# Optimization experiments

Measured on AMD Instinct MI355X. Metric: run time of the kernel, lower is better.

## Reference

```python
import jax, jax.numpy as jnp
import numpy as np

D = 20       # bond_dim (= virtual_dim = per-module output_dim)
BATCH = 128
BN_EPS = 1e-5


def _unfold(t, h, w, n):
    # torch x.unfold(2,h,h).unfold(3,w,w).reshape(b, C, -1, n)
    B, C, H, W = t.shape
    t = t.reshape(B, C, H // h, h, W // w, w).transpose(0, 1, 2, 4, 3, 5)
    return t.reshape(B, C, -1, n)


def _mps(x, cores, label):
    # x: [b, C, P, n] site values; cores: [P, n, D, F, D] with F = 2*C; label: [P, D, O, D]
    feat = jnp.concatenate([x, 1.0 - x], axis=1)              # [b, F, P, n]  ([x, 1-x] feature map)
    M = jnp.einsum('bfpn,pnufv->npbuv', feat, cores)           # [n, P, b, D, D] site matrices
    v = jnp.full((cores.shape[2],), cores.shape[2] ** -0.5, dtype=x.dtype)  # boundary vector
    left = jnp.einsum('u,pbuv->pbv', v, M[0])
    for i in range(1, M.shape[0]):                             # n is small & static (4 or 16)
        left = jnp.einsum('pbu,pbuv->pbv', left, M[i])
    return jnp.einsum('pbu,puov,v->bpo', left, label, v)       # [b, P, O]


def _bn(y, gamma, beta):
    # training-mode BatchNorm1d over channel axis 1 of [b, C, L]
    mean = y.mean(axis=(0, 2), keepdims=True)
    var = y.var(axis=(0, 2), keepdims=True)
    return (y - mean) * jax.lax.rsqrt(var + BN_EPS) * gamma[None, :, None] + beta[None, :, None]


def setup_inputs() -> dict:
    key = jax.random.key(0)
    ks = jax.random.split(key, 9)
    f32 = jnp.float32
    def core(k, shape):
        F = shape[-2]
        return (jax.random.normal(k, shape, f32) * np.float32(np.sqrt(3.0 / (D * F))))
    def lab(k, shape):
        return jax.random.normal(k, shape, f32) * np.float32(D ** -0.5)
    x = jax.random.uniform(ks[0], (BATCH, 48, 32, 32), f32)
    return {
        'x': x,
        'cores1': core(ks[1], (256, 4, D, 96, D)), 'label1': lab(ks[2], (256, D, D, D)),
        'g1': jnp.ones(256, f32), 'b1': jnp.zeros(256, f32),
        'cores2': core(ks[3], (64, 4, D, 2 * D, D)), 'label2': lab(ks[4], (64, D, D, D)),
        'g2': jnp.ones(64, f32), 'b2': jnp.zeros(64, f32),
        'cores3': core(ks[5], (16, 4, D, 2 * D, D)), 'label3': lab(ks[6], (16, D, D, D)),
        'g3': jnp.ones(16, f32), 'b3': jnp.zeros(16, f32),
        'coresF': core(ks[7], (16, D, 2 * D, D)), 'labelF': lab(ks[8], (D, 10, D)),
    }


def reference(x, cores1, label1, g1, b1, cores2, label2, g2, b2,
              cores3, label3, g3, b3, coresF, labelF):
    b = x.shape[0]
    # stage 1: 256 patch-experts over 4 sites each
    x1 = _unfold(x, 16, 16, 4)                  # [b, 48, 256, 4]
    y = _mps(x1, cores1, label1)                # [b, 256, D]
    y = _bn(y, g1, b1).reshape(b, D, 16, 16)    # faithful patch<->bond mixing view
    # stage 2: 64 experts
    y2 = _unfold(y, 8, 8, 4)                    # [b, D, 64, 4]
    y = _mps(y2, cores2, label2)                # [b, 64, D]
    y = _bn(y, g2, b2).reshape(b, D, 8, 8)
    # stage 3: 16 experts
    y3 = _unfold(y, 4, 4, 4)                    # [b, D, 16, 4]
    y = _mps(y3, cores3, label3)                # [b, 16, D]
    y = _bn(y, g3, b3)
    # final MPS over the 16 expert outputs (channels = D)
    y = y.transpose(0, 2, 1)[:, :, None, :]     # [b, D, 1, 16]
    out = _mps(y, coresF[None], labelF[None])   # [b, 1, 10]
    return out[:, 0, :]                         # squeeze -> [b, 10]
```

## Files before the change

kernel.cpp:

```cpp
#include <hip/hip_runtime.h>

#define VB 0.22360679774997896f

typedef __attribute__((ext_vector_type(8))) _Float16 half8;
typedef __attribute__((ext_vector_type(4))) float f32x4;

#define Z1_OFF   0
#define Z2_OFF   655360
#define Z3_OFF   819200
#define GS1_OFF  860160
#define GQ1_OFF  860416
#define GS2_OFF  860672
#define GQ2_OFF  860736
#define GS3_OFF  860800
#define GQ3_OFF  860816
#define LV1_OFF  860832
#define LV2_OFF  963232
#define LV3_OFF  988832
#define WH2_OFF  995232
#define WH3_OFF  4272032

#define WAVEBAR() __builtin_amdgcn_wave_barrier()

__global__ __launch_bounds__(256, 8)
void prep_kernel(const float* __restrict__ c2, const float* __restrict__ c3,
                 const float* __restrict__ l1, const float* __restrict__ l2,
                 const float* __restrict__ l3,
                 _Float16* __restrict__ Wh2, _Float16* __restrict__ Wh3,
                 float* __restrict__ v1, float* __restrict__ v2,
                 float* __restrict__ v3,
                 float* __restrict__ gzero)
{
    const int tid = threadIdx.x;
    const int b   = blockIdx.x;

    if (b < 4000) {
        int gidx = b * 256 + tid;
        int bb = gidx / 640;
        int o  = gidx - bb * 640;
        const float* src;
        _Float16* dst;
        if (bb < 1280) { src = c2 + (size_t)bb * 3200;          dst = Wh2 + (size_t)bb * 5120; }
        else           { src = c3 + (size_t)(bb - 1280) * 3200; dst = Wh3 + (size_t)(bb - 1280) * 5120; }
        int q  = o >> 6, l = o & 63;
        int ks = q / 5, nt = q - ks * 5;
        int c  = nt * 16 + (l & 15);
        int ul = c / 20;
        int v  = c - ul * 20;
        int f0 = ks * 32 + ((l >> 4) << 3);
        half8 hv;
        if (f0 < 40) {
            const float* sp = src + ul * 800 + f0 * 20 + v;
            #pragma unroll
            for (int j = 0; j < 8; ++j) hv[j] = (_Float16)sp[j * 20];
        } else {
            #pragma unroll
            for (int j = 0; j < 8; ++j) hv[j] = (_Float16)0.f;
        }
        *(half8*)(dst + (size_t)o * 8) = hv;
    } else if (b < 4336) {
        const int bb = b - 4000;
        const float* lb;
        float* ov;
        if (bb < 256)      { lb = l1 + (size_t)bb * 8000;         ov = v1 + bb * 400; }
        else if (bb < 320) { lb = l2 + (size_t)(bb - 256) * 8000; ov = v2 + (bb - 256) * 400; }
        else               { lb = l3 + (size_t)(bb - 320) * 8000; ov = v3 + (bb - 320) * 400; }
        for (int i = tid; i < 400; i += 256) {
            const float4* s = (const float4*)(lb + i * 20);
            float acc = 0.f;
            #pragma unroll
            for (int t = 0; t < 5; ++t) {
                float4 w = s[t];
                acc += w.x + w.y + w.z + w.w;
            }
            ov[i] = acc * VB;
        }
    } else {
        for (int i = tid; i < 672; i += 256) gzero[i] = 0.f;
    }
}

#define CHUNKX(ucv, LAST)                                                     \
    {                                                                         \
        if (!(LAST)) {                                                        \
            _Pragma("unroll")                                                 \
            for (int k = 0; k < 4; ++k) {                                     \
                int i4 = tid + k * 512;                                       \
                if (i4 < 1920) wr[k] = *(const float4*)(wnext + i4 * 4);      \
            }                                                                 \
            wnext += 7680;                                                    \
        }                                                                     \
        f32x4 acc[5];                                                         \
        _Pragma("unroll")                                                     \
        for (int nt = 0; nt < 5; ++nt) acc[nt] = (f32x4){0.f, 0.f, 0.f, 0.f};\
        _Pragma("unroll")                                                     \
        for (int ks = 0; ks < 3; ++ks) {                                      \
            _Pragma("unroll")                                                 \
            for (int nt = 0; nt < 5; ++nt) {                                  \
                half8 bf = *(const half8*)&Fcur[((ks * 5 + nt) * 64 + l) * 8];\
                acc[nt] = __builtin_amdgcn_mfma_f32_16x16x32_f16(             \
                    af[ks], bf, acc[nt], 0, 0, 0);                            \
            }                                                                 \
        }                                                                     \
        _Pragma("unroll")                                                     \
        for (int nt = 0; nt < 5; ++nt) {                                      \
            _Pragma("unroll")                                                 \
            for (int r = 0; r < 4; ++r)                                       \
                Mw[(hi * 4 + r) * 84 + nt * 16 + row16] = acc[nt][r];         \
        }                                                                     \
        WAVEBAR();                                                            \
        _Pragma("unroll")                                                     \
        for (int ul = 0; ul < 4; ++ul) {                                      \
            float lvx = lw[bQ * 20 + (ucv) * 4 + ul];                         \
            _Pragma("unroll")                                                 \
            for (int j = 0; j < 5; ++j)                                       \
                lacc[j] += lvx * Mw[bQ * 84 + ul * 20 + mh * 5 + j];          \
        }                                                                     \
        WAVEBAR();                                                            \
        __syncthreads();                                                      \
        if (!(LAST)) {                                                        \
            _Pragma("unroll")                                                 \
            for (int k = 0; k < 4; ++k) {                                     \
                int i4 = tid + k * 512;                                       \
                if (i4 < 1920) {                                              \
                    float vals[4] = {wr[k].x, wr[k].y, wr[k].z, wr[k].w};     \
                    _Pragma("unroll")                                         \
                    for (int t = 0; t < 4; ++t)                               \
                        Fnxt[sAddr[k][t]] = (_Float16)vals[t];                \
                }                                                             \
            }                                                                 \
        }                                                                     \
        __syncthreads();                                                      \
        { _Float16* t_ = Fcur; Fcur = Fnxt; Fnxt = t_; }                      \
    }

__global__ __launch_bounds__(512, 2)
void fused1_kernel(const float* __restrict__ x, const float* __restrict__ cores1,
                   const float* __restrict__ labv,
                   float* __restrict__ z1, float* __restrict__ gs, float* __restrict__ gq)
{
    __shared__ __align__(16) float xS[8 * 768];
    __shared__ __align__(16) _Float16 Fbuf[2][7680];
    __shared__ __align__(16) float MchunkS[8 * 16 * 84];
    __shared__ __align__(16) float leftS[8 * 320];
    __shared__ float redS[16];

    const int tid = threadIdx.x;
    const int bid = blockIdx.x;
    const int p   = (bid & 7) * 32 + (bid >> 3);
    const int wv  = tid >> 6, l = tid & 63;
    float* xSw = xS + wv * 768;
    float* Mw  = MchunkS + wv * 1344;
    float* lw  = leftS + wv * 320;
    const int row16 = l & 15, hi = l >> 4;
    const int bQ = l >> 2,   mh = l & 3;
    const int hh  = (p >> 7) * 16 + ((p >> 2) & 15);
    const int ww0 = ((p >> 6) & 1) * 16 + (p & 3) * 4;

    float4 xr[12];
    #pragma unroll
    for (int k = 0; k < 12; ++k) {
        int idx = l + k * 64;
        int br = idx / 48, c = idx - br * 48;
        xr[k] = *(const float4*)(x + (((size_t)((wv * 16 + br) * 48 + c)) << 10)
                                   + hh * 32 + ww0);
    }

    int sAddr[4][4];
    #pragma unroll
    for (int k = 0; k < 4; ++k) {
        int i4 = tid + k * 512;
        if (i4 < 1920) {
            #pragma unroll
            for (int t = 0; t < 4; ++t) {
                int e = i4 * 4 + t;
                int v = e % 20;
                int r = e / 20;
                int f = r % 96;
                int ul = r / 96;
                int c = ul * 20 + v;
                sAddr[k][t] = (((f >> 5) * 5 + (c >> 4)) * 64 +
                               ((f >> 3) & 3) * 16 + (c & 15)) * 8 + (f & 7);
            }
        }
    }

    #pragma unroll
    for (int j = 0; j < 5; ++j) lw[bQ * 20 + mh * 5 + j] = VB;
    WAVEBAR();

    float lacc[5] = {0.f, 0.f, 0.f, 0.f, 0.f};
    float4 wr[4];
    const float* wnext = cores1 + (size_t)p * 153600;

    #pragma unroll
    for (int k = 0; k < 4; ++k) {
        int i4 = tid + k * 512;
        if (i4 < 1920) wr[k] = *(const float4*)(wnext + i4 * 4);
    }
    wnext += 7680;
    _Float16* Fcur = &Fbuf[0][0];
    _Float16* Fnxt = &Fbuf[1][0];
    #pragma unroll
    for (int k = 0; k < 4; ++k) {
        int i4 = tid + k * 512;
        if (i4 < 1920) {
            float vals[4] = {wr[k].x, wr[k].y, wr[k].z, wr[k].w};
            #pragma unroll
            for (int t = 0; t < 4; ++t)
                Fcur[sAddr[k][t]] = (_Float16)vals[t];
        }
    }
    __syncthreads();

    #pragma unroll 1
    for (int n = 0; n < 4; ++n) {
        #pragma unroll
        for (int k = 0; k < 12; ++k) {
            int idx = l + k * 64;
            float v = (n == 0) ? xr[k].x : (n == 1) ? xr[k].y
                    : (n == 2) ? xr[k].z : xr[k].w;
            xSw[idx] = v;
        }
        WAVEBAR();
        half8 af[3];
        #pragma unroll
        for (int ks = 0; ks < 3; ++ks) {
            int f0 = ks * 32 + hi * 8;
            int cc = (f0 < 48) ? f0 : f0 - 48;
            float4 a  = *(const float4*)&xSw[row16 * 48 + cc];
            float4 b2 = *(const float4*)&xSw[row16 * 48 + cc + 4];
            float vv[8] = {a.x, a.y, a.z, a.w, b2.x, b2.y, b2.z, b2.w};
            bool inv = (f0 >= 48);
            half8 hv;
            #pragma unroll
            for (int j = 0; j < 8; ++j) hv[j] = (_Float16)(inv ? (1.f - vv[j]) : vv[j]);
            af[ks] = hv;
        }
        WAVEBAR();

        const bool last = (n == 3);
        CHUNKX(0, 0)
        CHUNKX(1, 0)
        CHUNKX(2, 0)
        CHUNKX(3, 0)
        CHUNKX(4, last)

        #pragma unroll
        for (int j = 0; j < 5; ++j) { lw[bQ * 20 + mh * 5 + j] = lacc[j]; lacc[j] = 0.f; }
        WAVEBAR();
    }

    const float* lvp = labv + p * 400;
    #pragma unroll
    for (int k = 0; k < 7; ++k) { int i = l + k * 64; if (i < 400) Mw[i] = lvp[i]; }
    WAVEBAR();
    float yv[5] = {0.f, 0.f, 0.f, 0.f, 0.f};
    #pragma unroll
    for (int u = 0; u < 20; ++u) {
        float lu = lw[bQ * 20 + u];
        #pragma unroll
        for (int j = 0; j < 5; ++j) yv[j] += lu * Mw[u * 20 + mh * 5 + j];
    }
    float s = 0.f, s2 = 0.f;
    #pragma unroll
    for (int j = 0; j < 5; ++j) {
        z1[(size_t)(wv * 16 + bQ) * 5120 + p * 20 + mh * 5 + j] = yv[j];
        s += yv[j]; s2 += yv[j] * yv[j];
    }
    #pragma unroll
    for (int off = 32; off > 0; off >>= 1) {
        s  += __shfl_down(s, off);
        s2 += __shfl_down(s2, off);
    }
    if (l == 0) { redS[wv] = s; redS[8 + wv] = s2; }
    __syncthreads();
    if (tid == 0) {
        float S = 0.f, Q = 0.f;
        #pragma unroll
        for (int w2 = 0; w2 < 8; ++w2) { S += redS[w2]; Q += redS[8 + w2]; }
        gs[p] = S; gq[p] = Q;
    }
}

#define UCBODYN(ucv, CUR, NXT)                                                   \
    {                                                                            \
        if ((ucv) < 4) {                                                         \
            const _Float16* bptr = whp + (size_t)((ucv) + 1) * 5120;             \
            _Pragma("unroll")                                                    \
            for (int q = 0; q < 10; ++q)                                         \
                NXT[q] = *(const half8*)(bptr + (q * 64 + l) * 8);               \
        }                                                                        \
        f32x4 acc[5];                                                            \
        _Pragma("unroll")                                                        \
        for (int nt = 0; nt < 5; ++nt) acc[nt] = (f32x4){0.f, 0.f, 0.f, 0.f};    \
        _Pragma("unroll")                                                        \
        for (int ks = 0; ks < 2; ++ks) {                                         \
            _Pragma("unroll")                                                    \
            for (int nt = 0; nt < 5; ++nt)                                       \
                acc[nt] = __builtin_amdgcn_mfma_f32_16x16x32_f16(                \
                    af[ks], CUR[ks * 5 + nt], acc[nt], 0, 0, 0);                 \
        }                                                                        \
        _Pragma("unroll")                                                        \
        for (int nt = 0; nt < 5; ++nt) {                                         \
            _Pragma("unroll")                                                    \
            for (int r = 0; r < 4; ++r)                                          \
                Mw[(hi * 4 + r) * 84 + nt * 16 + row16] = acc[nt][r];            \
        }                                                                        \
        WAVEBAR();                                                               \
        _Pragma("unroll")                                                        \
        for (int ul = 0; ul < 4; ++ul) {                                         \
            float lvx = lw[bQ * 20 + (ucv) * 4 + ul];                            \
            _Pragma("unroll")                                                    \
            for (int j = 0; j < 5; ++j)                                          \
                lacc[j] += lvx * Mw[bQ * 84 + ul * 20 + mh * 5 + j];             \
        }                                                                        \
        WAVEBAR();                                                               \
    }

template <int STAGE>
__global__ __launch_bounds__(256, 2)
void fusedN_kernel(const float* __restrict__ zin, const _Float16* __restrict__ Wh,
                   const float* __restrict__ labv,
                   const float* __restrict__ gsin, const float* __restrict__ gqin,
                   const float* __restrict__ gam,  const float* __restrict__ bet,
                   float* __restrict__ zout,
                   float* __restrict__ gsout, float* __restrict__ gqout)
{
    constexpr int ZIN  = (STAGE == 2) ? 5120 : 1280;
    constexpr int ZOUT = (STAGE == 2) ? 1280 : 320;
    constexpr int JUMP = (STAGE == 2) ? 256 : 64;

    __shared__ __align__(16) float zS[4 * 320];
    __shared__ float scS[4 * 20], shS[4 * 20];
    __shared__ __align__(16) float MchunkS[4 * 16 * 84];
    __shared__ __align__(16) float leftS[4 * 320];

    const int tid = threadIdx.x;
    const int p   = blockIdx.x;
    const int bh  = blockIdx.y;
    const int wv  = tid >> 6, l = tid & 63;
    float* zSw = zS + wv * 320;
    float* scw = scS + wv * 20;
    float* shw = shS + wv * 20;
    float* Mw  = MchunkS + wv * 1344;
    float* lw  = leftS + wv * 320;
    const int row16 = l & 15, hi = l >> 4;
    const int bQ = l >> 2,   mh = l & 3;
    const int bg = bh * 64;

    #pragma unroll
    for (int j = 0; j < 5; ++j) lw[bQ * 20 + mh * 5 + j] = VB;
    WAVEBAR();

    float lacc[5] = {0.f, 0.f, 0.f, 0.f, 0.f};

    #pragma unroll 1
    for (int n = 0; n < 4; ++n) {
        int hh, ww;
        if (STAGE == 2) { hh = (p >> 5) * 8 + ((p >> 1) & 7); ww = ((p >> 4) & 1) * 8 + (p & 1) * 4 + n; }
        else            { hh = (p >> 3) * 4 + (p & 3);        ww = ((p >> 2) & 1) * 4 + n; }
        const int oo = (STAGE == 2) ? (hh * 16 + ww) : (hh * 8 + ww);

        if (l < 20) {
            int ch = (l * JUMP + oo) / 20;
            float mean = gsin[ch] * (1.f / 2560.f);
            float var  = gqin[ch] * (1.f / 2560.f) - mean * mean;
            float rstd = rsqrtf(var + 1e-5f);
            float sc = gam[ch] * rstd;
            scw[l] = sc;
            shw[l] = bet[ch] - mean * sc;
        }
        WAVEBAR();
        #pragma unroll
        for (int q = 0; q < 5; ++q) {
            int d = hi * 5 + q;
            float zraw = zin[(size_t)(bg + wv * 16 + row16) * ZIN + d * JUMP + oo];
            zSw[row16 * 20 + d] = zraw * scw[d] + shw[d];
        }
        WAVEBAR();
        half8 af[2];
        #pragma unroll
        for (int ks = 0; ks < 2; ++ks) {
            int f0 = ks * 32 + hi * 8;
            half8 hv;
            #pragma unroll
            for (int j = 0; j < 8; ++j) {
                int f = f0 + j;
                float val;
                if (f < 20)      val = zSw[row16 * 20 + f];
                else if (f < 40) val = 1.f - zSw[row16 * 20 + f - 20];
                else             val = 0.f;
                hv[j] = (_Float16)val;
            }
            af[ks] = hv;
        }
        WAVEBAR();

        const _Float16* whp = Wh + (size_t)((p * 4 + n) * 5) * 5120;
        half8 bA[10], bB[10];
        {
            #pragma unroll
            for (int q = 0; q < 10; ++q) bA[q] = *(const half8*)(whp + (q * 64 + l) * 8);
        }
        UCBODYN(0, bA, bB)
        UCBODYN(1, bB, bA)
        UCBODYN(2, bA, bB)
        UCBODYN(3, bB, bA)
        UCBODYN(4, bA, bB)

        #pragma unroll
        for (int j = 0; j < 5; ++j) { lw[bQ * 20 + mh * 5 + j] = lacc[j]; lacc[j] = 0.f; }
        WAVEBAR();
    }

    const float* lvp = labv + p * 400;
    #pragma unroll
    for (int k = 0; k < 7; ++k) { int i = l + k * 64; if (i < 400) Mw[i] = lvp[i]; }
    WAVEBAR();
    float yv[5] = {0.f, 0.f, 0.f, 0.f, 0.f};
    #pragma unroll
    for (int u = 0; u < 20; ++u) {
        float lu = lw[bQ * 20 + u];
        #pragma unroll
        for (int j = 0; j < 5; ++j) yv[j] += lu * Mw[u * 20 + mh * 5 + j];
    }
    float s = 0.f, s2 = 0.f;
    #pragma unroll
    for (int j = 0; j < 5; ++j) {
        zout[(size_t)(bg + wv * 16 + bQ) * ZOUT + p * 20 + mh * 5 + j] = yv[j];
        s += yv[j]; s2 += yv[j] * yv[j];
    }
    #pragma unroll
    for (int off = 32; off > 0; off >>= 1) {
        s  += __shfl_down(s, off);
        s2 += __shfl_down(s2, off);
    }
    if (l == 0) { atomicAdd(&gsout[p], s); atomicAdd(&gqout[p], s2); }
}

__global__ __launch_bounds__(256, 4)
void final_kernel(const float* __restrict__ z3,
                  const float* __restrict__ coresF,
                  const float* __restrict__ labelF,
                  const float* __restrict__ g3,
                  const float* __restrict__ b3,
                  const float* __restrict__ gsum3,
                  const float* __restrict__ gsq3,
                  float* __restrict__ out)
{
    __shared__ __align__(16) float fS[16 * 40];
    __shared__ __align__(16) float MS[16 * 400];
    __shared__ float lvS[200];
    __shared__ float scS[16], shS[16];
    __shared__ float leftS[20];

    const int b   = blockIdx.x;
    const int tid = threadIdx.x;

    if (tid < 16) {
        float mean = gsum3[tid] * (1.f / 2560.f);
        float var  = gsq3[tid] * (1.f / 2560.f) - mean * mean;
        float rstd = rsqrtf(var + 1e-5f);
        float sc   = g3[tid] * rstd;
        scS[tid] = sc;
        shS[tid] = b3[tid] - mean * sc;
    }
    __syncthreads();

    for (int i = tid; i < 640; i += 256) {
        int n = i / 40, f = i - n * 40;
        float raw = z3[(size_t)b * 320 + n * 20 + (f % 20)];
        float val = raw * scS[n] + shS[n];
        fS[i] = (f < 20) ? val : (1.f - val);
    }
    for (int i = tid; i < 200; i += 256) {
        int u = i / 10, o = i - u * 10;
        const float* lb = labelF + (size_t)(u * 10 + o) * 20;
        float s = 0.f;
        #pragma unroll
        for (int vv = 0; vv < 20; ++vv) s += lb[vv];
        lvS[i] = s * VB;
    }
    __syncthreads();

    for (int i = tid; i < 6400; i += 256) {
        int n = i / 400, uv = i - n * 400;
        int u = uv / 20, v = uv - u * 20;
        const float* wb = coresF + ((size_t)(n * 20 + u) * 40) * 20 + v;
        const float* fb = fS + n * 40;
        float acc = 0.f;
        #pragma unroll
        for (int f = 0; f < 40; ++f) acc += fb[f] * wb[f * 20];
        MS[i] = acc;
    }
    __syncthreads();

    if (tid < 64) {
        if (tid < 20) leftS[tid] = VB;
        WAVEBAR();
        #pragma unroll 1
        for (int n = 0; n < 16; ++n) {
            float tmp = 0.f;
            if (tid < 20) {
                #pragma unroll
                for (int u = 0; u < 20; ++u) tmp += leftS[u] * MS[n * 400 + u * 20 + tid];
            }
            WAVEBAR();
            if (tid < 20) leftS[tid] = tmp;
            WAVEBAR();
        }
        if (tid < 10) {
            float s = 0.f;
            #pragma unroll
            for (int u = 0; u < 20; ++u) s += leftS[u] * lvS[u * 10 + tid];
            out[b * 10 + tid] = s;
        }
    }
}

extern "C" void kernel_launch(void* const* d_in, const int* in_sizes, int n_in,
                              void* d_out, int out_size, void* d_ws, size_t ws_size,
                              hipStream_t stream)
{
    const float* x      = (const float*)d_in[0];
    const float* cores1 = (const float*)d_in[1];
    const float* label1 = (const float*)d_in[2];
    const float* g1     = (const float*)d_in[3];
    const float* b1     = (const float*)d_in[4];
    const float* cores2 = (const float*)d_in[5];
    const float* label2 = (const float*)d_in[6];
    const float* g2     = (const float*)d_in[7];
    const float* b2     = (const float*)d_in[8];
    const float* cores3 = (const float*)d_in[9];
    const float* label3 = (const float*)d_in[10];
    const float* g3     = (const float*)d_in[11];
    const float* b3     = (const float*)d_in[12];
    const float* coresF = (const float*)d_in[13];
    const float* labelF = (const float*)d_in[14];

    float* ws  = (float*)d_ws;
    float* z1  = ws + Z1_OFF;
    float* z2  = ws + Z2_OFF;
    float* z3  = ws + Z3_OFF;
    float* gs1 = ws + GS1_OFF; float* gq1 = ws + GQ1_OFF;
    float* gs2 = ws + GS2_OFF; float* gq2 = ws + GQ2_OFF;
    float* gs3 = ws + GS3_OFF; float* gq3 = ws + GQ3_OFF;
    float* lv1 = ws + LV1_OFF;
    float* lv2 = ws + LV2_OFF;
    float* lv3 = ws + LV3_OFF;
    _Float16* Wh2 = (_Float16*)(ws + WH2_OFF);
    _Float16* Wh3 = (_Float16*)(ws + WH3_OFF);

    prep_kernel<<<4337, 256, 0, stream>>>(cores2, cores3,
                                          label1, label2, label3,
                                          Wh2, Wh3,
                                          lv1, lv2, lv3, gs1);

    fused1_kernel<<<256, 512, 0, stream>>>(x, cores1, lv1, z1, gs1, gq1);
    fusedN_kernel<2><<<dim3(64, 2), 256, 0, stream>>>(z1, Wh2, lv2, gs1, gq1, g1, b1,
                                                      z2, gs2, gq2);
    fusedN_kernel<3><<<dim3(16, 2), 256, 0, stream>>>(z2, Wh3, lv3, gs2, gq2, g2, b2,
                                                      z3, gs3, gq3);
    final_kernel<<<128, 256, 0, stream>>>(z3, coresF, labelF, g3, b3,
                                          gs3, gq3, (float*)d_out);
}
```

Baseline: 113.0 us.

## Drop prep kernel; convert cores to fp16 in-kernel and fuse label reductions

The separate prep kernel, which converted stage-2/3 cores to fp16 MFMA layout and pre-reduced the label vectors, is removed. The stage-N kernels now use 512 threads per block, covering the whole batch in one block. They stream fp32 cores through a double-buffered LDS fp16 tile, as fused1 does, and each computes its label vector in LDS. BN statistics are reduced per block instead of with atomics, which also removes the need to zero them. This saves one launch and the global round-trip for the converted weights, at the cost of fewer blocks in stages 2/3 and extra per-chunk block barriers.

```diff
diff --git a/kernel.cpp b/kernel.cpp
--- a/kernel.cpp
+++ b/kernel.cpp
@@ -14,71 +14,8 @@
 #define GQ2_OFF  860736
 #define GS3_OFF  860800
 #define GQ3_OFF  860816
-#define LV1_OFF  860832
-#define LV2_OFF  963232
-#define LV3_OFF  988832
-#define WH2_OFF  995232
-#define WH3_OFF  4272032
 
 #define WAVEBAR() __builtin_amdgcn_wave_barrier()
-
-__global__ __launch_bounds__(256, 8)
-void prep_kernel(const float* __restrict__ c2, const float* __restrict__ c3,
-                 const float* __restrict__ l1, const float* __restrict__ l2,
-                 const float* __restrict__ l3,
-                 _Float16* __restrict__ Wh2, _Float16* __restrict__ Wh3,
-                 float* __restrict__ v1, float* __restrict__ v2,
-                 float* __restrict__ v3,
-                 float* __restrict__ gzero)
-{
-    const int tid = threadIdx.x;
-    const int b   = blockIdx.x;
-
-    if (b < 4000) {
-        int gidx = b * 256 + tid;
-        int bb = gidx / 640;
-        int o  = gidx - bb * 640;
-        const float* src;
-        _Float16* dst;
-        if (bb < 1280) { src = c2 + (size_t)bb * 3200;          dst = Wh2 + (size_t)bb * 5120; }
-        else           { src = c3 + (size_t)(bb - 1280) * 3200; dst = Wh3 + (size_t)(bb - 1280) * 5120; }
-        int q  = o >> 6, l = o & 63;
-        int ks = q / 5, nt = q - ks * 5;
-        int c  = nt * 16 + (l & 15);
-        int ul = c / 20;
-        int v  = c - ul * 20;
-        int f0 = ks * 32 + ((l >> 4) << 3);
-        half8 hv;
-        if (f0 < 40) {
-            const float* sp = src + ul * 800 + f0 * 20 + v;
-            #pragma unroll
-            for (int j = 0; j < 8; ++j) hv[j] = (_Float16)sp[j * 20];
-        } else {
-            #pragma unroll
-            for (int j = 0; j < 8; ++j) hv[j] = (_Float16)0.f;
-        }
-        *(half8*)(dst + (size_t)o * 8) = hv;
-    } else if (b < 4336) {
-        const int bb = b - 4000;
-        const float* lb;
-        float* ov;
-        if (bb < 256)      { lb = l1 + (size_t)bb * 8000;         ov = v1 + bb * 400; }
-        else if (bb < 320) { lb = l2 + (size_t)(bb - 256) * 8000; ov = v2 + (bb - 256) * 400; }
-        else               { lb = l3 + (size_t)(bb - 320) * 8000; ov = v3 + (bb - 320) * 400; }
-        for (int i = tid; i < 400; i += 256) {
-            const float4* s = (const float4*)(lb + i * 20);
-            float acc = 0.f;
-            #pragma unroll
-            for (int t = 0; t < 5; ++t) {
-                float4 w = s[t];
-                acc += w.x + w.y + w.z + w.w;
-            }
-            ov[i] = acc * VB;
-        }
-    } else {
-        for (int i = tid; i < 672; i += 256) gzero[i] = 0.f;
-    }
-}
 
 #define CHUNKX(ucv, LAST)                                                     \
     {                                                                         \
@@ -136,13 +73,14 @@
 
 __global__ __launch_bounds__(512, 2)
 void fused1_kernel(const float* __restrict__ x, const float* __restrict__ cores1,
-                   const float* __restrict__ labv,
+                   const float* __restrict__ label1,
                    float* __restrict__ z1, float* __restrict__ gs, float* __restrict__ gq)
 {
     __shared__ __align__(16) float xS[8 * 768];
     __shared__ __align__(16) _Float16 Fbuf[2][7680];
     __shared__ __align__(16) float MchunkS[8 * 16 * 84];
     __shared__ __align__(16) float leftS[8 * 320];
+    __shared__ __align__(16) float labvS[400];
     __shared__ float redS[16];
 
     const int tid = threadIdx.x;
@@ -213,6 +151,14 @@
     }
     __syncthreads();
 
+    if (tid < 400) {
+        const float* lb = label1 + (size_t)p * 8000 + tid * 20;
+        float s = 0.f;
+        #pragma unroll
+        for (int vv = 0; vv < 20; ++vv) s += lb[vv];
+        labvS[tid] = s * VB;
+    }
+
     #pragma unroll 1
     for (int n = 0; n < 4; ++n) {
         #pragma unroll
@@ -251,16 +197,12 @@
         WAVEBAR();
     }
 
-    const float* lvp = labv + p * 400;
-    #pragma unroll
-    for (int k = 0; k < 7; ++k) { int i = l + k * 64; if (i < 400) Mw[i] = lvp[i]; }
-    WAVEBAR();
     float yv[5] = {0.f, 0.f, 0.f, 0.f, 0.f};
     #pragma unroll
     for (int u = 0; u < 20; ++u) {
         float lu = lw[bQ * 20 + u];
         #pragma unroll
-        for (int j = 0; j < 5; ++j) yv[j] += lu * Mw[u * 20 + mh * 5 + j];
+        for (int j = 0; j < 5; ++j) yv[j] += lu * labvS[u * 20 + mh * 5 + j];
     }
     float s = 0.f, s2 = 0.f;
     #pragma unroll
@@ -283,45 +225,64 @@
     }
 }
 
-#define UCBODYN(ucv, CUR, NXT)                                                   \
-    {                                                                            \
-        if ((ucv) < 4) {                                                         \
-            const _Float16* bptr = whp + (size_t)((ucv) + 1) * 5120;             \
-            _Pragma("unroll")                                                    \
-            for (int q = 0; q < 10; ++q)                                         \
-                NXT[q] = *(const half8*)(bptr + (q * 64 + l) * 8);               \
-        }                                                                        \
-        f32x4 acc[5];                                                            \
-        _Pragma("unroll")                                                        \
-        for (int nt = 0; nt < 5; ++nt) acc[nt] = (f32x4){0.f, 0.f, 0.f, 0.f};    \
-        _Pragma("unroll")                                                        \
-        for (int ks = 0; ks < 2; ++ks) {                                         \
-            _Pragma("unroll")                                                    \
-            for (int nt = 0; nt < 5; ++nt)                                       \
-                acc[nt] = __builtin_amdgcn_mfma_f32_16x16x32_f16(                \
-                    af[ks], CUR[ks * 5 + nt], acc[nt], 0, 0, 0);                 \
-        }                                                                        \
-        _Pragma("unroll")                                                        \
-        for (int nt = 0; nt < 5; ++nt) {                                         \
-            _Pragma("unroll")                                                    \
-            for (int r = 0; r < 4; ++r)                                          \
-                Mw[(hi * 4 + r) * 84 + nt * 16 + row16] = acc[nt][r];            \
-        }                                                                        \
-        WAVEBAR();                                                               \
-        _Pragma("unroll")                                                        \
-        for (int ul = 0; ul < 4; ++ul) {                                         \
-            float lvx = lw[bQ * 20 + (ucv) * 4 + ul];                            \
-            _Pragma("unroll")                                                    \
-            for (int j = 0; j < 5; ++j)                                          \
-                lacc[j] += lvx * Mw[bQ * 84 + ul * 20 + mh * 5 + j];             \
-        }                                                                        \
-        WAVEBAR();                                                               \
+#define CHUNKN(ucv_abs, LAST)                                                 \
+    {                                                                         \
+        if (!(LAST)) {                                                        \
+            _Pragma("unroll")                                                 \
+            for (int k = 0; k < 2; ++k) {                                     \
+                int i4 = tid + k * 512;                                       \
+                if (i4 < 800) wr[k] = *(const float4*)(wnext + i4 * 4);       \
+            }                                                                 \
+            wnext += 3200;                                                    \
+        }                                                                     \
+        f32x4 acc[5];                                                         \
+        _Pragma("unroll")                                                     \
+        for (int nt = 0; nt < 5; ++nt) acc[nt] = (f32x4){0.f, 0.f, 0.f, 0.f};\
+        _Pragma("unroll")                                                     \
+        for (int ks = 0; ks < 2; ++ks) {                                      \
+            _Pragma("unroll")                                                 \
+            for (int nt = 0; nt < 5; ++nt) {                                  \
+                half8 bf = *(const half8*)&Fcur[((ks * 5 + nt) * 64 + l) * 8];\
+                acc[nt] = __builtin_amdgcn_mfma_f32_16x16x32_f16(             \
+                    af[ks], bf, acc[nt], 0, 0, 0);                            \
+            }                                                                 \
+        }                                                                     \
+        _Pragma("unroll")                                                     \
+        for (int nt = 0; nt < 5; ++nt) {                                      \
+            _Pragma("unroll")                                                 \
+            for (int r = 0; r < 4; ++r)                                       \
+                Mw[(hi * 4 + r) * 84 + nt * 16 + row16] = acc[nt][r];         \
+        }                                                                     \
+        WAVEBAR();                                                            \
+        _Pragma("unroll")                                                     \
+        for (int ul = 0; ul < 4; ++ul) {                                      \
+            float lvx = lw[bQ * 20 + ((ucv_abs) % 5) * 4 + ul];               \
+            _Pragma("unroll")                                                 \
+            for (int j = 0; j < 5; ++j)                                       \
+                lacc[j] += lvx * Mw[bQ * 84 + ul * 20 + mh * 5 + j];          \
+        }                                                                     \
+        WAVEBAR();                                                            \
+        __syncthreads();                                                      \
+        if (!(LAST)) {                                                        \
+            _Pragma("unroll")                                                 \
+            for (int k = 0; k < 2; ++k) {                                     \
+                int i4 = tid + k * 512;                                       \
+                if (i4 < 800) {                                               \
+                    float vals[4] = {wr[k].x, wr[k].y, wr[k].z, wr[k].w};     \
+                    _Pragma("unroll")                                         \
+                    for (int t = 0; t < 4; ++t)                               \
+                        Fnxt[sAddr2[k][t]] = (_Float16)vals[t];               \
+                }                                                             \
+            }                                                                 \
+        }                                                                     \
+        __syncthreads();                                                      \
+        { _Float16* t_ = Fcur; Fcur = Fnxt; Fnxt = t_; }                      \
     }
 
 template <int STAGE>
-__global__ __launch_bounds__(256, 2)
-void fusedN_kernel(const float* __restrict__ zin, const _Float16* __restrict__ Wh,
-                   const float* __restrict__ labv,
+__global__ __launch_bounds__(512, 2)
+void stageN_kernel(const float* __restrict__ zin, const float* __restrict__ cores,
+                   const float* __restrict__ label,
                    const float* __restrict__ gsin, const float* __restrict__ gqin,
                    const float* __restrict__ gam,  const float* __restrict__ bet,
                    float* __restrict__ zout,
@@ -331,15 +292,18 @@
     constexpr int ZOUT = (STAGE == 2) ? 1280 : 320;
     constexpr int JUMP = (STAGE == 2) ? 256 : 64;
 
-    __shared__ __align__(16) float zS[4 * 320];
-    __shared__ float scS[4 * 20], shS[4 * 20];
-    __shared__ __align__(16) float MchunkS[4 * 16 * 84];
-    __shared__ __align__(16) float leftS[4 * 320];
+    __shared__ __align__(16) float zS[8 * 320];
+    __shared__ float scS[8 * 20], shS[8 * 20];
+    __shared__ __align__(16) _Float16 Fbuf[2][5120];
+    __shared__ __align__(16) float MchunkS[8 * 16 * 84];
+    __shared__ __align__(16) float leftS[8 * 320];
+    __shared__ __align__(16) float labvS[400];
+    __shared__ float redS[16];
 
     const int tid = threadIdx.x;
     const int p   = blockIdx.x;
-    const int bh  = blockIdx.y;
     const int wv  = tid >> 6, l = tid & 63;
+    const int bh  = wv >> 2, wvl = wv & 3;
     float* zSw = zS + wv * 320;
     float* scw = scS + wv * 20;
     float* shw = shS + wv * 20;
@@ -347,7 +311,62 @@
     float* lw  = leftS + wv * 320;
     const int row16 = l & 15, hi = l >> 4;
     const int bQ = l >> 2,   mh = l & 3;
-    const int bg = bh * 64;
+    const int bg = bh * 64 + wvl * 16;
+
+    int sAddr2[2][4];
+    #pragma unroll
+    for (int k = 0; k < 2; ++k) {
+        int i4 = tid + k * 512;
+        if (i4 < 800) {
+            #pragma unroll
+            for (int t = 0; t < 4; ++t) {
+                int e = i4 * 4 + t;
+                int v = e % 20;
+                int r = e / 20;
+                int f = r % 40;
+                int ul = r / 40;
+                int c = ul * 20 + v;
+                sAddr2[k][t] = (((f >> 5) * 5 + (c >> 4)) * 64 +
+                                ((f >> 3) & 3) * 16 + (c & 15)) * 8 + (f & 7);
+            }
+        }
+    }
+
+    #pragma unroll
+    for (int k = 0; k < 3; ++k) {
+        int i = tid + k * 512;
+        if (i < 1280) ((uint4*)&Fbuf[0][0])[i] = (uint4){0, 0, 0, 0};
+    }
+    if (tid < 400) {
+        const float* lb = label + (size_t)p * 8000 + tid * 20;
+        float s = 0.f;
+        #pragma unroll
+        for (int vv = 0; vv < 20; ++vv) s += lb[vv];
+        labvS[tid] = s * VB;
+    }
+    __syncthreads();
+
+    float4 wr[2];
+    const float* wnext = cores + (size_t)p * 64000;
+    #pragma unroll
+    for (int k = 0; k < 2; ++k) {
+        int i4 = tid + k * 512;
+        if (i4 < 800) wr[k] = *(const float4*)(wnext + i4 * 4);
+    }
+    wnext += 3200;
+    _Float16* Fcur = &Fbuf[0][0];
+    _Float16* Fnxt = &Fbuf[1][0];
+    #pragma unroll
+    for (int k = 0; k < 2; ++k) {
+        int i4 = tid + k * 512;
+        if (i4 < 800) {
+            float vals[4] = {wr[k].x, wr[k].y, wr[k].z, wr[k].w};
+            #pragma unroll
+            for (int t = 0; t < 4; ++t)
+                Fcur[sAddr2[k][t]] = (_Float16)vals[t];
+        }
+    }
+    __syncthreads();
 
     #pragma unroll
     for (int j = 0; j < 5; ++j) lw[bQ * 20 + mh * 5 + j] = VB;
@@ -375,7 +394,7 @@
         #pragma unroll
         for (int q = 0; q < 5; ++q) {
             int d = hi * 5 + q;
-            float zraw = zin[(size_t)(bg + wv * 16 + row16) * ZIN + d * JUMP + oo];
+            float zraw = zin[(size_t)(bg + row16) * ZIN + d * JUMP + oo];
             zSw[row16 * 20 + d] = zraw * scw[d] + shw[d];
         }
         WAVEBAR();
@@ -397,38 +416,29 @@
         }
         WAVEBAR();
 
-        const _Float16* whp = Wh + (size_t)((p * 4 + n) * 5) * 5120;
-        half8 bA[10], bB[10];
-        {
-            #pragma unroll
-            for (int q = 0; q < 10; ++q) bA[q] = *(const half8*)(whp + (q * 64 + l) * 8);
-        }
-        UCBODYN(0, bA, bB)
-        UCBODYN(1, bB, bA)
-        UCBODYN(2, bA, bB)
-        UCBODYN(3, bB, bA)
-        UCBODYN(4, bA, bB)
+        const int c0 = n * 5;
+        CHUNKN(c0 + 0, 0)
+        CHUNKN(c0 + 1, 0)
+        CHUNKN(c0 + 2, 0)
+        CHUNKN(c0 + 3, 0)
+        CHUNKN(c0 + 4, (n == 3))
 
         #pragma unroll
         for (int j = 0; j < 5; ++j) { lw[bQ * 20 + mh * 5 + j] = lacc[j]; lacc[j] = 0.f; }
         WAVEBAR();
     }
 
-    const float* lvp = labv + p * 400;
-    #pragma unroll
-    for (int k = 0; k < 7; ++k) { int i = l + k * 64; if (i < 400) Mw[i] = lvp[i]; }
-    WAVEBAR();
     float yv[5] = {0.f, 0.f, 0.f, 0.f, 0.f};
     #pragma unroll
     for (int u = 0; u < 20; ++u) {
         float lu = lw[bQ * 20 + u];
         #pragma unroll
-        for (int j = 0; j < 5; ++j) yv[j] += lu * Mw[u * 20 + mh * 5 + j];
+        for (int j = 0; j < 5; ++j) yv[j] += lu * labvS[u * 20 + mh * 5 + j];
     }
     float s = 0.f, s2 = 0.f;
     #pragma unroll
     for (int j = 0; j < 5; ++j) {
-        zout[(size_t)(bg + wv * 16 + bQ) * ZOUT + p * 20 + mh * 5 + j] = yv[j];
+        zout[(size_t)(bg + bQ) * ZOUT + p * 20 + mh * 5 + j] = yv[j];
         s += yv[j]; s2 += yv[j] * yv[j];
     }
     #pragma unroll
@@ -436,10 +446,17 @@
         s  += __shfl_down(s, off);
         s2 += __shfl_down(s2, off);
     }
-    if (l == 0) { atomicAdd(&gsout[p], s); atomicAdd(&gqout[p], s2); }
+    if (l == 0) { redS[wv] = s; redS[8 + wv] = s2; }
+    __syncthreads();
+    if (tid == 0) {
+        float S = 0.f, Q = 0.f;
+        #pragma unroll
+        for (int w2 = 0; w2 < 8; ++w2) { S += redS[w2]; Q += redS[8 + w2]; }
+        gsout[p] = S; gqout[p] = Q;
+    }
 }
 
-__global__ __launch_bounds__(256, 4)
+__global__ __launch_bounds__(512, 2)
 void final_kernel(const float* __restrict__ z3,
                   const float* __restrict__ coresF,
                   const float* __restrict__ labelF,
@@ -468,13 +485,13 @@
     }
     __syncthreads();
 
-    for (int i = tid; i < 640; i += 256) {
+    for (int i = tid; i < 640; i += 512) {
         int n = i / 40, f = i - n * 40;
         float raw = z3[(size_t)b * 320 + n * 20 + (f % 20)];
         float val = raw * scS[n] + shS[n];
         fS[i] = (f < 20) ? val : (1.f - val);
     }
-    for (int i = tid; i < 200; i += 256) {
+    for (int i = tid; i < 200; i += 512) {
         int u = i / 10, o = i - u * 10;
         const float* lb = labelF + (size_t)(u * 10 + o) * 20;
         float s = 0.f;
@@ -484,7 +501,7 @@
     }
     __syncthreads();
 
-    for (int i = tid; i < 6400; i += 256) {
+    for (int i = tid; i < 6400; i += 512) {
         int n = i / 400, uv = i - n * 400;
         int u = uv / 20, v = uv - u * 20;
         const float* wb = coresF + ((size_t)(n * 20 + u) * 40) * 20 + v;
@@ -546,22 +563,14 @@
     float* gs1 = ws + GS1_OFF; float* gq1 = ws + GQ1_OFF;
     float* gs2 = ws + GS2_OFF; float* gq2 = ws + GQ2_OFF;
     float* gs3 = ws + GS3_OFF; float* gq3 = ws + GQ3_OFF;
-    float* lv1 = ws + LV1_OFF;
-    float* lv2 = ws + LV2_OFF;
-    float* lv3 = ws + LV3_OFF;
-    _Float16* Wh2 = (_Float16*)(ws + WH2_OFF);
-    _Float16* Wh3 = (_Float16*)(ws + WH3_OFF);
-
-    prep_kernel<<<4337, 256, 0, stream>>>(cores2, cores3,
-                                          label1, label2, label3,
-                                          Wh2, Wh3,
-                                          lv1, lv2, lv3, gs1);
-
-    fused1_kernel<<<256, 512, 0, stream>>>(x, cores1, lv1, z1, gs1, gq1);
-    fusedN_kernel<2><<<dim3(64, 2), 256, 0, stream>>>(z1, Wh2, lv2, gs1, gq1, g1, b1,
-                                                      z2, gs2, gq2);
-    fusedN_kernel<3><<<dim3(16, 2), 256, 0, stream>>>(z2, Wh3, lv3, gs2, gq2, g2, b2,
-                                                      z3, gs3, gq3);
-    final_kernel<<<128, 256, 0, stream>>>(z3, coresF, labelF, g3, b3,
+
+    fused1_kernel<<<256, 512, 0, stream>>>(x, cores1, label1, z1, gs1, gq1);
+    stageN_kernel<2><<<64, 512, 0, stream>>>(z1, cores2, label2,
+                                             gs1, gq1, g1, b1,
+                                             z2, gs2, gq2);
+    stageN_kernel<3><<<16, 512, 0, stream>>>(z2, cores3, label3,
+                                             gs2, gq2, g2, b2,
+                                             z3, gs3, gq3);
+    final_kernel<<<128, 512, 0, stream>>>(z3, coresF, labelF, g3, b3,
                                           gs3, gq3, (float*)d_out);
 }
```

Result: slower. 132.2 us (+17.0%).

## Prefetch stage-1 core chunks two ahead and repack stage-2/3 weights via LDS

Applied to the files above, without the earlier changes.

In the stage-1 fused kernel, the core-weight chunk loads now use two register buffers and are issued two chunks ahead, with all 20 chunks unrolled across four site macros. The goal is to hide global-load latency behind the MFMA work. The prep kernel now gives each 3200-element core slice to one block: it reads the slice with coalesced float4 loads, scatters it into a fragment layout in LDS, then writes it out with coalesced stores, replacing strided per-element gathers. The cost is higher register pressure from the extra prefetch buffer and larger unrolled code; the kernel rename and atomic-lane test rewrite are cosmetic.

```diff
diff --git a/kernel.cpp b/kernel.cpp
--- a/kernel.cpp
+++ b/kernel.cpp
@@ -31,35 +31,49 @@
                  float* __restrict__ v3,
                  float* __restrict__ gzero)
 {
+    __shared__ __align__(16) _Float16 fragS[5120];
     const int tid = threadIdx.x;
     const int b   = blockIdx.x;
 
-    if (b < 4000) {
-        int gidx = b * 256 + tid;
-        int bb = gidx / 640;
-        int o  = gidx - bb * 640;
+    if (b < 1600) {
         const float* src;
         _Float16* dst;
-        if (bb < 1280) { src = c2 + (size_t)bb * 3200;          dst = Wh2 + (size_t)bb * 5120; }
-        else           { src = c3 + (size_t)(bb - 1280) * 3200; dst = Wh3 + (size_t)(bb - 1280) * 5120; }
-        int q  = o >> 6, l = o & 63;
-        int ks = q / 5, nt = q - ks * 5;
-        int c  = nt * 16 + (l & 15);
-        int ul = c / 20;
-        int v  = c - ul * 20;
-        int f0 = ks * 32 + ((l >> 4) << 3);
-        half8 hv;
-        if (f0 < 40) {
-            const float* sp = src + ul * 800 + f0 * 20 + v;
-            #pragma unroll
-            for (int j = 0; j < 8; ++j) hv[j] = (_Float16)sp[j * 20];
-        } else {
-            #pragma unroll
-            for (int j = 0; j < 8; ++j) hv[j] = (_Float16)0.f;
-        }
-        *(half8*)(dst + (size_t)o * 8) = hv;
-    } else if (b < 4336) {
-        const int bb = b - 4000;
+        if (b < 1280) { src = c2 + (size_t)b * 3200;          dst = Wh2 + (size_t)b * 5120; }
+        else          { src = c3 + (size_t)(b - 1280) * 3200; dst = Wh3 + (size_t)(b - 1280) * 5120; }
+        #pragma unroll
+        for (int k = 0; k < 3; ++k) {
+            int i = tid + k * 256;
+            if (i < 640) ((uint4*)fragS)[i] = (uint4){0, 0, 0, 0};
+        }
+        __syncthreads();
+        #pragma unroll
+        for (int k = 0; k < 4; ++k) {
+            int i4 = tid + k * 256;
+            if (i4 < 800) {
+                float4 w = *(const float4*)(src + i4 * 4);
+                float vals[4] = {w.x, w.y, w.z, w.w};
+                #pragma unroll
+                for (int t = 0; t < 4; ++t) {
+                    int e = i4 * 4 + t;
+                    int v = e % 20;
+                    int r = e / 20;
+                    int f = r % 40;
+                    int ul = r / 40;
+                    int c = ul * 20 + v;
+                    int addr = (((f >> 5) * 5 + (c >> 4)) * 64 +
+                                ((f >> 3) & 3) * 16 + (c & 15)) * 8 + (f & 7);
+                    fragS[addr] = (_Float16)vals[t];
+                }
+            }
+        }
+        __syncthreads();
+        #pragma unroll
+        for (int k = 0; k < 3; ++k) {
+            int i = tid + k * 256;
+            if (i < 640) ((uint4*)dst)[i] = ((const uint4*)fragS)[i];
+        }
+    } else if (b < 1936) {
+        const int bb = b - 1600;
         const float* lb;
         float* ov;
         if (bb < 256)      { lb = l1 + (size_t)bb * 8000;         ov = v1 + bb * 400; }
@@ -80,16 +94,32 @@
     }
 }
 
-#define CHUNKX(ucv, LAST)                                                     \
+#define LOADW(W, ci)                                                          \
     {                                                                         \
-        if (!(LAST)) {                                                        \
-            _Pragma("unroll")                                                 \
-            for (int k = 0; k < 4; ++k) {                                     \
-                int i4 = tid + k * 512;                                       \
-                if (i4 < 1920) wr[k] = *(const float4*)(wnext + i4 * 4);      \
+        const float* wp_ = wbase + (size_t)(ci) * 7680;                       \
+        _Pragma("unroll")                                                     \
+        for (int k = 0; k < 4; ++k) {                                         \
+            int i4 = tid + k * 512;                                           \
+            if (i4 < 1920) W[k] = *(const float4*)(wp_ + i4 * 4);             \
+        }                                                                     \
+    }
+
+#define SCATW(W, DST)                                                         \
+    {                                                                         \
+        _Pragma("unroll")                                                     \
+        for (int k = 0; k < 4; ++k) {                                         \
+            int i4 = tid + k * 512;                                           \
+            if (i4 < 1920) {                                                  \
+                float vals[4] = {W[k].x, W[k].y, W[k].z, W[k].w};             \
+                _Pragma("unroll")                                             \
+                for (int t = 0; t < 4; ++t)                                   \
+                    DST[sAddr[k][t]] = (_Float16)vals[t];                     \
             }                                                                 \
-            wnext += 7680;                                                    \
-        }                                                                     \
+        }                                                                     \
+    }
+
+#define CHUNKD(ci, W)                                                         \
+    {                                                                         \
         f32x4 acc[5];                                                         \
         _Pragma("unroll")                                                     \
         for (int nt = 0; nt < 5; ++nt) acc[nt] = (f32x4){0.f, 0.f, 0.f, 0.f};\
@@ -111,27 +141,55 @@
         WAVEBAR();                                                            \
         _Pragma("unroll")                                                     \
         for (int ul = 0; ul < 4; ++ul) {                                      \
-            float lvx = lw[bQ * 20 + (ucv) * 4 + ul];                         \
+            float lvx = lw[bQ * 20 + ((ci) % 5) * 4 + ul];                    \
             _Pragma("unroll")                                                 \
             for (int j = 0; j < 5; ++j)                                       \
                 lacc[j] += lvx * Mw[bQ * 84 + ul * 20 + mh * 5 + j];          \
         }                                                                     \
         WAVEBAR();                                                            \
         __syncthreads();                                                      \
-        if (!(LAST)) {                                                        \
-            _Pragma("unroll")                                                 \
-            for (int k = 0; k < 4; ++k) {                                     \
-                int i4 = tid + k * 512;                                       \
-                if (i4 < 1920) {                                              \
-                    float vals[4] = {wr[k].x, wr[k].y, wr[k].z, wr[k].w};     \
-                    _Pragma("unroll")                                         \
-                    for (int t = 0; t < 4; ++t)                               \
-                        Fnxt[sAddr[k][t]] = (_Float16)vals[t];                \
-                }                                                             \
-            }                                                                 \
-        }                                                                     \
+        if ((ci) < 19) { SCATW(W, Fnxt) }                                     \
         __syncthreads();                                                      \
         { _Float16* t_ = Fcur; Fcur = Fnxt; Fnxt = t_; }                      \
+        if ((ci) <= 16) { LOADW(W, (ci) + 3) }                                \
+    }
+
+#define SITE(nv, W0, W1, W2, W3, W4)                                          \
+    {                                                                         \
+        _Pragma("unroll")                                                     \
+        for (int k = 0; k < 12; ++k) {                                        \
+            int idx = l + k * 64;                                             \
+            float v = ((nv) == 0) ? xr[k].x : ((nv) == 1) ? xr[k].y           \
+                    : ((nv) == 2) ? xr[k].z : xr[k].w;                        \
+            xSw[idx] = v;                                                     \
+        }                                                                     \
+        WAVEBAR();                                                            \
+        half8 af[3];                                                          \
+        _Pragma("unroll")                                                     \
+        for (int ks = 0; ks < 3; ++ks) {                                      \
+            int f0 = ks * 32 + hi * 8;                                        \
+            int cc = (f0 < 48) ? f0 : f0 - 48;                                \
+            float4 a  = *(const float4*)&xSw[row16 * 48 + cc];                \
+            float4 b2 = *(const float4*)&xSw[row16 * 48 + cc + 4];            \
+            float vv[8] = {a.x, a.y, a.z, a.w, b2.x, b2.y, b2.z, b2.w};       \
+            bool inv = (f0 >= 48);                                            \
+            half8 hv;                                                         \
+            _Pragma("unroll")                                                 \
+            for (int j = 0; j < 8; ++j)                                       \
+                hv[j] = (_Float16)(inv ? (1.f - vv[j]) : vv[j]);              \
+            af[ks] = hv;                                                      \
+        }                                                                     \
+        WAVEBAR();                                                            \
+        CHUNKD((nv) * 5 + 0, W0)                                              \
+        CHUNKD((nv) * 5 + 1, W1)                                              \
+        CHUNKD((nv) * 5 + 2, W2)                                              \
+        CHUNKD((nv) * 5 + 3, W3)                                              \
+        CHUNKD((nv) * 5 + 4, W4)                                              \
+        _Pragma("unroll")                                                     \
+        for (int j = 0; j < 5; ++j) {                                         \
+            lw[bQ * 20 + mh * 5 + j] = lacc[j]; lacc[j] = 0.f;                \
+        }                                                                     \
+        WAVEBAR();                                                            \
     }
 
 __global__ __launch_bounds__(512, 2)
@@ -190,66 +248,22 @@
     WAVEBAR();
 
     float lacc[5] = {0.f, 0.f, 0.f, 0.f, 0.f};
-    float4 wr[4];
-    const float* wnext = cores1 + (size_t)p * 153600;
-
-    #pragma unroll
-    for (int k = 0; k < 4; ++k) {
-        int i4 = tid + k * 512;
-        if (i4 < 1920) wr[k] = *(const float4*)(wnext + i4 * 4);
-    }
-    wnext += 7680;
+    float4 wrA[4], wrB[4];
+    const float* wbase = cores1 + (size_t)p * 153600;
+
     _Float16* Fcur = &Fbuf[0][0];
     _Float16* Fnxt = &Fbuf[1][0];
-    #pragma unroll
-    for (int k = 0; k < 4; ++k) {
-        int i4 = tid + k * 512;
-        if (i4 < 1920) {
-            float vals[4] = {wr[k].x, wr[k].y, wr[k].z, wr[k].w};
-            #pragma unroll
-            for (int t = 0; t < 4; ++t)
-                Fcur[sAddr[k][t]] = (_Float16)vals[t];
-        }
-    }
+
+    LOADW(wrA, 0)
+    SCATW(wrA, Fcur)
+    LOADW(wrA, 1)
+    LOADW(wrB, 2)
     __syncthreads();
 
-    #pragma unroll 1
-    for (int n = 0; n < 4; ++n) {
-        #pragma unroll
-        for (int k = 0; k < 12; ++k) {
-            int idx = l + k * 64;
-            float v = (n == 0) ? xr[k].x : (n == 1) ? xr[k].y
-                    : (n == 2) ? xr[k].z : xr[k].w;
-            xSw[idx] = v;
-        }
-        WAVEBAR();
-        half8 af[3];
-        #pragma unroll
-        for (int ks = 0; ks < 3; ++ks) {
-            int f0 = ks * 32 + hi * 8;
-            int cc = (f0 < 48) ? f0 : f0 - 48;
-            float4 a  = *(const float4*)&xSw[row16 * 48 + cc];
-            float4 b2 = *(const float4*)&xSw[row16 * 48 + cc + 4];
-            float vv[8] = {a.x, a.y, a.z, a.w, b2.x, b2.y, b2.z, b2.w};
-            bool inv = (f0 >= 48);
-            half8 hv;
-            #pragma unroll
-            for (int j = 0; j < 8; ++j) hv[j] = (_Float16)(inv ? (1.f - vv[j]) : vv[j]);
-            af[ks] = hv;
-        }
-        WAVEBAR();
-
-        const bool last = (n == 3);
-        CHUNKX(0, 0)
-        CHUNKX(1, 0)
-        CHUNKX(2, 0)
-        CHUNKX(3, 0)
-        CHUNKX(4, last)
-
-        #pragma unroll
-        for (int j = 0; j < 5; ++j) { lw[bQ * 20 + mh * 5 + j] = lacc[j]; lacc[j] = 0.f; }
-        WAVEBAR();
-    }
+    SITE(0, wrA, wrB, wrA, wrB, wrA)
+    SITE(1, wrB, wrA, wrB, wrA, wrB)
+    SITE(2, wrA, wrB, wrA, wrB, wrA)
+    SITE(3, wrB, wrA, wrB, wrA, wrB)
 
     const float* lvp = labv + p * 400;
     #pragma unroll
@@ -320,7 +334,7 @@
 
 template <int STAGE>
 __global__ __launch_bounds__(256, 2)
-void fusedN_kernel(const float* __restrict__ zin, const _Float16* __restrict__ Wh,
+void stageN_kernel(const float* __restrict__ zin, const _Float16* __restrict__ Wh,
                    const float* __restrict__ labv,
                    const float* __restrict__ gsin, const float* __restrict__ gqin,
                    const float* __restrict__ gam,  const float* __restrict__ bet,
@@ -436,7 +450,10 @@
         s  += __shfl_down(s, off);
         s2 += __shfl_down(s2, off);
     }
-    if (l == 0) { atomicAdd(&gsout[p], s); atomicAdd(&gqout[p], s2); }
+    if ((tid & 63) == 0) {
+        atomicAdd(&gsout[p], s);
+        atomicAdd(&gqout[p], s2);
+    }
 }
 
 __global__ __launch_bounds__(256, 4)
@@ -552,15 +569,15 @@
     _Float16* Wh2 = (_Float16*)(ws + WH2_OFF);
     _Float16* Wh3 = (_Float16*)(ws + WH3_OFF);
 
-    prep_kernel<<<4337, 256, 0, stream>>>(cores2, cores3,
+    prep_kernel<<<1937, 256, 0, stream>>>(cores2, cores3,
                                           label1, label2, label3,
                                           Wh2, Wh3,
                                           lv1, lv2, lv3, gs1);
 
     fused1_kernel<<<256, 512, 0, stream>>>(x, cores1, lv1, z1, gs1, gq1);
-    fusedN_kernel<2><<<dim3(64, 2), 256, 0, stream>>>(z1, Wh2, lv2, gs1, gq1, g1, b1,
+    stageN_kernel<2><<<dim3(64, 2), 256, 0, stream>>>(z1, Wh2, lv2, gs1, gq1, g1, b1,
                                                       z2, gs2, gq2);
-    fusedN_kernel<3><<<dim3(16, 2), 256, 0, stream>>>(z2, Wh3, lv3, gs2, gq2, g2, b2,
+    stageN_kernel<3><<<dim3(16, 2), 256, 0, stream>>>(z2, Wh3, lv3, gs2, gq2, g2, b2,
                                                       z3, gs3, gq3);
     final_kernel<<<128, 256, 0, stream>>>(z3, coresF, labelF, g3, b3,
                                           gs3, gq3, (float*)d_out);
```

New measurement: 110.5 us. 1.02x faster.
